# Performance work log

Hardware: AMD Instinct MI355X
Metric: run time of the kernel (lower is better)

## Reference

```python
import jax, jax.numpy as jnp
import numpy as np

NUM_LABELS = 10000
HIDDEN = 1024
B = 256
K = 4096


def setup_inputs() -> dict:
    key = jax.random.key(0)
    k1, k2, k3, k4, k5, k6 = jax.random.split(key, 6)
    embeddings = jax.random.normal(k1, (B, HIDDEN), dtype=jnp.float32)
    W1 = jax.random.normal(k2, (NUM_LABELS, 8, HIDDEN), dtype=jnp.float32) * 0.02
    b1 = jax.random.normal(k3, (NUM_LABELS, 8), dtype=jnp.float32) * 0.02
    W2 = jax.random.normal(k4, (NUM_LABELS, 1, 8), dtype=jnp.float32) * 0.02
    b2 = jax.random.normal(k5, (NUM_LABELS, 1), dtype=jnp.float32) * 0.02
    task_ids = jax.random.randint(k6, (K,), 0, NUM_LABELS, dtype=jnp.int64)
    return {"embeddings": embeddings, "W1": W1, "b1": b1, "W2": W2, "b2": b2, "task_ids": task_ids}


def reference(embeddings, W1, b1, W2, b2, task_ids):
    # Gather the selected heads (irregular access over the 10k-head tables).
    w1 = W1[task_ids]      # [K, 8, H]
    bb1 = b1[task_ids]     # [K, 8]
    w2 = W2[task_ids]      # [K, 1, 8]
    bb2 = b2[task_ids]     # [K, 1]
    # Batched tiny MLP: Linear(H,8) -> ReLU -> Linear(8,1), grouped over K heads.
    h = jax.nn.relu(jnp.einsum('bh,koh->kbo', embeddings, w1) + bb1[:, None, :])  # [K, B, 8]
    out = jnp.einsum('kbo,kio->kbi', h, w2) + bb2[:, None, :]                     # [K, B, 1]
    # torch: cat([head(emb).squeeze(-1) for ...], dim=-1) -> flat [K*B], task-major.
    return out[..., 0].reshape(-1)
```

## Files before the change

### kernel.cpp

```cpp
#include <hip/hip_runtime.h>

#define HID 1024
#define BATCH 256
#define KTASK 4096
#define TPB 8
#define NCOL (TPB * 8)
#define KC 32
#define NSTEPS (HID / KC)
#define STRIDE 80

typedef __bf16 bf16x8 __attribute__((ext_vector_type(8)));
typedef __bf16 bf16x4 __attribute__((ext_vector_type(4)));
typedef float f32x4 __attribute__((ext_vector_type(4)));

static __device__ __forceinline__ bf16x4 cvt4(const float4& a) {
    bf16x4 r;
    r[0] = (__bf16)a.x; r[1] = (__bf16)a.y; r[2] = (__bf16)a.z; r[3] = (__bf16)a.w;
    return r;
}

__global__ __launch_bounds__(256, 4)
void cvt_emb_kernel(const float* __restrict__ emb, __bf16* __restrict__ dst) {
    int i = (blockIdx.x * 256 + threadIdx.x) * 4;
    float4 v = *(const float4*)(emb + i);
    *(bf16x4*)(dst + i) = cvt4(v);
}

__global__ __launch_bounds__(512, 4)
void mtc_kernel(const __bf16* __restrict__ embb, const float* __restrict__ W1,
                const float* __restrict__ b1, const float* __restrict__ W2,
                const float* __restrict__ b2, const int* __restrict__ tids,
                float* __restrict__ out)
{
    __shared__ __align__(16) char wbuf[2][NCOL * STRIDE];

    const int t = threadIdx.x;
    const int lane = t & 63;
    const int w = t >> 6;
    const int blk = blockIdx.x;

    const int srow = t >> 3;
    const int sq   = t & 7;
    const int stask = tids[blk * TPB + (srow >> 3)];
    const float* sgp = W1 + (size_t)stask * (8 * HID) + (size_t)(srow & 7) * HID + sq * 4;
    char* const swr0 = &wbuf[0][0] + srow * STRIDE + sq * 8;
    char* const swr1 = swr0 + NCOL * STRIDE;

    const __bf16* agp = embb + (size_t)(w * 32 + (lane & 15)) * HID + (lane >> 4) * 8;
    const int boff = (lane & 15) * STRIDE + (lane >> 4) * 16;
    const char* const rb0 = &wbuf[0][0];
    const char* const rb1 = &wbuf[1][0];

    f32x4 acc[2][4];
    const f32x4 zero = {0.f, 0.f, 0.f, 0.f};
#pragma unroll
    for (int i = 0; i < 2; ++i)
#pragma unroll
        for (int j = 0; j < 4; ++j) acc[i][j] = zero;

    float4 wa = *(const float4*)(sgp);
    bf16x8 acur0 = *(const bf16x8*)(agp);
    bf16x8 acur1 = *(const bf16x8*)(agp + 16 * HID);
    *(bf16x4*)swr0 = cvt4(wa);
    float4 wb = *(const float4*)(sgp + KC);
    __syncthreads();

    for (int i = 0; i < 15; ++i) {
        const int s = 2 * i;
        {
            wa = *(const float4*)(sgp + (s + 2) * KC);
            bf16x8 an0 = *(const bf16x8*)(agp + (s + 1) * KC);
            bf16x8 an1 = *(const bf16x8*)(agp + (s + 1) * KC + 16 * HID);
#pragma unroll
            for (int nt = 0; nt < 4; ++nt) {
                bf16x8 bf = *(const bf16x8*)(rb0 + nt * (16 * STRIDE) + boff);
                acc[0][nt] = __builtin_amdgcn_mfma_f32_16x16x32_bf16(acur0, bf, acc[0][nt], 0, 0, 0);
                acc[1][nt] = __builtin_amdgcn_mfma_f32_16x16x32_bf16(acur1, bf, acc[1][nt], 0, 0, 0);
            }
            *(bf16x4*)swr1 = cvt4(wb);
            acur0 = an0; acur1 = an1;
            __syncthreads();
        }
        {
            wb = *(const float4*)(sgp + (s + 3) * KC);
            bf16x8 an0 = *(const bf16x8*)(agp + (s + 2) * KC);
            bf16x8 an1 = *(const bf16x8*)(agp + (s + 2) * KC + 16 * HID);
#pragma unroll
            for (int nt = 0; nt < 4; ++nt) {
                bf16x8 bf = *(const bf16x8*)(rb1 + nt * (16 * STRIDE) + boff);
                acc[0][nt] = __builtin_amdgcn_mfma_f32_16x16x32_bf16(acur0, bf, acc[0][nt], 0, 0, 0);
                acc[1][nt] = __builtin_amdgcn_mfma_f32_16x16x32_bf16(acur1, bf, acc[1][nt], 0, 0, 0);
            }
            *(bf16x4*)swr0 = cvt4(wa);
            acur0 = an0; acur1 = an1;
            __syncthreads();
        }
    }
    {
        bf16x8 an0 = *(const bf16x8*)(agp + 31 * KC);
        bf16x8 an1 = *(const bf16x8*)(agp + 31 * KC + 16 * HID);
#pragma unroll
        for (int nt = 0; nt < 4; ++nt) {
            bf16x8 bf = *(const bf16x8*)(rb0 + nt * (16 * STRIDE) + boff);
            acc[0][nt] = __builtin_amdgcn_mfma_f32_16x16x32_bf16(acur0, bf, acc[0][nt], 0, 0, 0);
            acc[1][nt] = __builtin_amdgcn_mfma_f32_16x16x32_bf16(acur1, bf, acc[1][nt], 0, 0, 0);
        }
        *(bf16x4*)swr1 = cvt4(wb);
        acur0 = an0; acur1 = an1;
        __syncthreads();
    }
    {
#pragma unroll
        for (int nt = 0; nt < 4; ++nt) {
            bf16x8 bf = *(const bf16x8*)(rb1 + nt * (16 * STRIDE) + boff);
            acc[0][nt] = __builtin_amdgcn_mfma_f32_16x16x32_bf16(acur0, bf, acc[0][nt], 0, 0, 0);
            acc[1][nt] = __builtin_amdgcn_mfma_f32_16x16x32_bf16(acur1, bf, acc[1][nt], 0, 0, 0);
        }
    }

    const int col = lane & 15;
    const int rgrp = lane >> 4;
    const int o = col & 7;
#pragma unroll
    for (int nt = 0; nt < 4; ++nt) {
        const int tl = nt * 2 + (col >> 3);
        const int task = tids[blk * TPB + tl];
        const float bb1 = b1[task * 8 + o];
        const float ww2 = W2[task * 8 + o];
#pragma unroll
        for (int bt = 0; bt < 2; ++bt) {
            float v[4];
#pragma unroll
            for (int r = 0; r < 4; ++r) {
                float x = acc[bt][nt][r] + bb1;
                x = x > 0.f ? x : 0.f;
                v[r] = x * ww2;
            }
#pragma unroll
            for (int m = 1; m <= 4; m <<= 1) {
#pragma unroll
                for (int r = 0; r < 4; ++r) v[r] += __shfl_xor(v[r], m, 64);
            }
            if ((lane & 7) == 0) {
                const float bb2 = b2[task];
                const int brow = w * 32 + bt * 16 + rgrp * 4;
                float4 o4 = make_float4(v[0] + bb2, v[1] + bb2, v[2] + bb2, v[3] + bb2);
                *(float4*)(out + (size_t)(blk * TPB + tl) * BATCH + brow) = o4;
            }
        }
    }
}

extern "C" void kernel_launch(void* const* d_in, const int* in_sizes, int n_in,
                              void* d_out, int out_size, void* d_ws, size_t ws_size,
                              hipStream_t stream) {
    const float* emb = (const float*)d_in[0];
    const float* W1  = (const float*)d_in[1];
    const float* b1  = (const float*)d_in[2];
    const float* W2  = (const float*)d_in[3];
    const float* b2  = (const float*)d_in[4];
    const int*   tid = (const int*)d_in[5];
    float* outp = (float*)d_out;
    __bf16* embb = (__bf16*)d_ws;

    cvt_emb_kernel<<<dim3(BATCH * HID / (256 * 4)), dim3(256), 0, stream>>>(emb, embb);
    mtc_kernel<<<dim3(KTASK / TPB), dim3(512), 0, stream>>>(embb, W1, b1, W2, b2, tid, outp);
}
```

Measured before the change: 50.09 us.

## Double K-chunk to 64 with triple-register prefetch pipeline for W1 staging

Widens each K step from 32 to 64 columns, halving the number of barriers and LDS stages, and has each thread load and convert 8 floats per step instead of 4. W1 global loads are now issued three steps ahead through a rotating set of three register buffers, and embedding fragments are loaded directly each step instead of being prefetched one step ahead. The aim is to expose more memory-level parallelism for the gathered W1 stream and cut synchronisation overhead. In exchange it needs more registers and a larger LDS footprint (144-byte stride), which could reduce occupancy.

```diff
diff --git a/kernel.cpp b/kernel.cpp
--- a/kernel.cpp
+++ b/kernel.cpp
@@ -4,18 +4,20 @@
 #define BATCH 256
 #define KTASK 4096
 #define TPB 8
-#define NCOL (TPB * 8)
-#define KC 32
-#define NSTEPS (HID / KC)
-#define STRIDE 80
+#define NCOL 64
+#define KC 64
+#define NSTEPS 16
+#define STRIDE 144
+#define BUFSZ (NCOL * STRIDE)
 
 typedef __bf16 bf16x8 __attribute__((ext_vector_type(8)));
 typedef __bf16 bf16x4 __attribute__((ext_vector_type(4)));
 typedef float f32x4 __attribute__((ext_vector_type(4)));
 
-static __device__ __forceinline__ bf16x4 cvt4(const float4& a) {
-    bf16x4 r;
+static __device__ __forceinline__ bf16x8 cvt8(const float4& a, const float4& b) {
+    bf16x8 r;
     r[0] = (__bf16)a.x; r[1] = (__bf16)a.y; r[2] = (__bf16)a.z; r[3] = (__bf16)a.w;
+    r[4] = (__bf16)b.x; r[5] = (__bf16)b.y; r[6] = (__bf16)b.z; r[7] = (__bf16)b.w;
     return r;
 }
 
@@ -23,7 +25,9 @@
 void cvt_emb_kernel(const float* __restrict__ emb, __bf16* __restrict__ dst) {
     int i = (blockIdx.x * 256 + threadIdx.x) * 4;
     float4 v = *(const float4*)(emb + i);
-    *(bf16x4*)(dst + i) = cvt4(v);
+    bf16x4 r;
+    r[0] = (__bf16)v.x; r[1] = (__bf16)v.y; r[2] = (__bf16)v.z; r[3] = (__bf16)v.w;
+    *(bf16x4*)(dst + i) = r;
 }
 
 __global__ __launch_bounds__(512, 4)
@@ -32,7 +36,7 @@
                 const float* __restrict__ b2, const int* __restrict__ tids,
                 float* __restrict__ out)
 {
-    __shared__ __align__(16) char wbuf[2][NCOL * STRIDE];
+    __shared__ __align__(16) char wbuf[2 * BUFSZ];
 
     const int t = threadIdx.x;
     const int lane = t & 63;
@@ -42,14 +46,11 @@
     const int srow = t >> 3;
     const int sq   = t & 7;
     const int stask = tids[blk * TPB + (srow >> 3)];
-    const float* sgp = W1 + (size_t)stask * (8 * HID) + (size_t)(srow & 7) * HID + sq * 4;
-    char* const swr0 = &wbuf[0][0] + srow * STRIDE + sq * 8;
-    char* const swr1 = swr0 + NCOL * STRIDE;
+    const float* sgp = W1 + (size_t)stask * (8 * HID) + (size_t)(srow & 7) * HID + sq * 8;
+    char* const swr = &wbuf[0] + srow * STRIDE + sq * 16;
 
     const __bf16* agp = embb + (size_t)(w * 32 + (lane & 15)) * HID + (lane >> 4) * 8;
     const int boff = (lane & 15) * STRIDE + (lane >> 4) * 16;
-    const char* const rb0 = &wbuf[0][0];
-    const char* const rb1 = &wbuf[1][0];
 
     f32x4 acc[2][4];
     const f32x4 zero = {0.f, 0.f, 0.f, 0.f};
@@ -58,65 +59,68 @@
 #pragma unroll
         for (int j = 0; j < 4; ++j) acc[i][j] = zero;
 
-    float4 wa = *(const float4*)(sgp);
-    bf16x8 acur0 = *(const bf16x8*)(agp);
-    bf16x8 acur1 = *(const bf16x8*)(agp + 16 * HID);
-    *(bf16x4*)swr0 = cvt4(wa);
-    float4 wb = *(const float4*)(sgp + KC);
+    float4 qa0 = *(const float4*)(sgp);
+    float4 qa1 = *(const float4*)(sgp + 4);
+    *(bf16x8*)swr = cvt8(qa0, qa1);
+    float4 qb0 = *(const float4*)(sgp + 1 * KC);
+    float4 qb1 = *(const float4*)(sgp + 1 * KC + 4);
+    float4 qc0 = *(const float4*)(sgp + 2 * KC);
+    float4 qc1 = *(const float4*)(sgp + 2 * KC + 4);
     __syncthreads();
 
-    for (int i = 0; i < 15; ++i) {
-        const int s = 2 * i;
-        {
-            wa = *(const float4*)(sgp + (s + 2) * KC);
-            bf16x8 an0 = *(const bf16x8*)(agp + (s + 1) * KC);
-            bf16x8 an1 = *(const bf16x8*)(agp + (s + 1) * KC + 16 * HID);
-#pragma unroll
-            for (int nt = 0; nt < 4; ++nt) {
-                bf16x8 bf = *(const bf16x8*)(rb0 + nt * (16 * STRIDE) + boff);
-                acc[0][nt] = __builtin_amdgcn_mfma_f32_16x16x32_bf16(acur0, bf, acc[0][nt], 0, 0, 0);
-                acc[1][nt] = __builtin_amdgcn_mfma_f32_16x16x32_bf16(acur1, bf, acc[1][nt], 0, 0, 0);
-            }
-            *(bf16x4*)swr1 = cvt4(wb);
-            acur0 = an0; acur1 = an1;
-            __syncthreads();
-        }
-        {
-            wb = *(const float4*)(sgp + (s + 3) * KC);
-            bf16x8 an0 = *(const bf16x8*)(agp + (s + 2) * KC);
-            bf16x8 an1 = *(const bf16x8*)(agp + (s + 2) * KC + 16 * HID);
-#pragma unroll
-            for (int nt = 0; nt < 4; ++nt) {
-                bf16x8 bf = *(const bf16x8*)(rb1 + nt * (16 * STRIDE) + boff);
-                acc[0][nt] = __builtin_amdgcn_mfma_f32_16x16x32_bf16(acur0, bf, acc[0][nt], 0, 0, 0);
-                acc[1][nt] = __builtin_amdgcn_mfma_f32_16x16x32_bf16(acur1, bf, acc[1][nt], 0, 0, 0);
-            }
-            *(bf16x4*)swr0 = cvt4(wa);
-            acur0 = an0; acur1 = an1;
-            __syncthreads();
-        }
+#define STEP(S, QW0, QW1, QI0, QI1, RB, WB, ISSUE, WRITE, BAR)                              \
+    {                                                                                       \
+        bf16x8 a00 = *(const bf16x8*)(agp + (S) * KC);                                      \
+        bf16x8 a01 = *(const bf16x8*)(agp + (S) * KC + 32);                                 \
+        bf16x8 a10 = *(const bf16x8*)(agp + (S) * KC + 16 * HID);                           \
+        bf16x8 a11 = *(const bf16x8*)(agp + (S) * KC + 16 * HID + 32);                      \
+        if (ISSUE) {                                                                        \
+            QI0 = *(const float4*)(sgp + ((S) + 3) * KC);                                   \
+            QI1 = *(const float4*)(sgp + ((S) + 3) * KC + 4);                               \
+        }                                                                                   \
+        const char* rb = &wbuf[0] + (RB) * BUFSZ;                                           \
+        bf16x8 b00 = *(const bf16x8*)(rb + 0 * (16 * STRIDE) + boff);                       \
+        bf16x8 b01 = *(const bf16x8*)(rb + 0 * (16 * STRIDE) + boff + 64);                  \
+        bf16x8 b10 = *(const bf16x8*)(rb + 1 * (16 * STRIDE) + boff);                       \
+        bf16x8 b11 = *(const bf16x8*)(rb + 1 * (16 * STRIDE) + boff + 64);                  \
+        bf16x8 b20 = *(const bf16x8*)(rb + 2 * (16 * STRIDE) + boff);                       \
+        bf16x8 b21 = *(const bf16x8*)(rb + 2 * (16 * STRIDE) + boff + 64);                  \
+        bf16x8 b30 = *(const bf16x8*)(rb + 3 * (16 * STRIDE) + boff);                       \
+        bf16x8 b31 = *(const bf16x8*)(rb + 3 * (16 * STRIDE) + boff + 64);                  \
+        if (WRITE) *(bf16x8*)(swr + (WB) * BUFSZ) = cvt8(QW0, QW1);                         \
+        acc[0][0] = __builtin_amdgcn_mfma_f32_16x16x32_bf16(a00, b00, acc[0][0], 0, 0, 0);  \
+        acc[0][1] = __builtin_amdgcn_mfma_f32_16x16x32_bf16(a00, b10, acc[0][1], 0, 0, 0);  \
+        acc[0][2] = __builtin_amdgcn_mfma_f32_16x16x32_bf16(a00, b20, acc[0][2], 0, 0, 0);  \
+        acc[0][3] = __builtin_amdgcn_mfma_f32_16x16x32_bf16(a00, b30, acc[0][3], 0, 0, 0);  \
+        acc[1][0] = __builtin_amdgcn_mfma_f32_16x16x32_bf16(a10, b00, acc[1][0], 0, 0, 0);  \
+        acc[1][1] = __builtin_amdgcn_mfma_f32_16x16x32_bf16(a10, b10, acc[1][1], 0, 0, 0);  \
+        acc[1][2] = __builtin_amdgcn_mfma_f32_16x16x32_bf16(a10, b20, acc[1][2], 0, 0, 0);  \
+        acc[1][3] = __builtin_amdgcn_mfma_f32_16x16x32_bf16(a10, b30, acc[1][3], 0, 0, 0);  \
+        acc[0][0] = __builtin_amdgcn_mfma_f32_16x16x32_bf16(a01, b01, acc[0][0], 0, 0, 0);  \
+        acc[0][1] = __builtin_amdgcn_mfma_f32_16x16x32_bf16(a01, b11, acc[0][1], 0, 0, 0);  \
+        acc[0][2] = __builtin_amdgcn_mfma_f32_16x16x32_bf16(a01, b21, acc[0][2], 0, 0, 0);  \
+        acc[0][3] = __builtin_amdgcn_mfma_f32_16x16x32_bf16(a01, b31, acc[0][3], 0, 0, 0);  \
+        acc[1][0] = __builtin_amdgcn_mfma_f32_16x16x32_bf16(a11, b01, acc[1][0], 0, 0, 0);  \
+        acc[1][1] = __builtin_amdgcn_mfma_f32_16x16x32_bf16(a11, b11, acc[1][1], 0, 0, 0);  \
+        acc[1][2] = __builtin_amdgcn_mfma_f32_16x16x32_bf16(a11, b21, acc[1][2], 0, 0, 0);  \
+        acc[1][3] = __builtin_amdgcn_mfma_f32_16x16x32_bf16(a11, b31, acc[1][3], 0, 0, 0);  \
+        if (BAR) __syncthreads();                                                           \
     }
-    {
-        bf16x8 an0 = *(const bf16x8*)(agp + 31 * KC);
-        bf16x8 an1 = *(const bf16x8*)(agp + 31 * KC + 16 * HID);
-#pragma unroll
-        for (int nt = 0; nt < 4; ++nt) {
-            bf16x8 bf = *(const bf16x8*)(rb0 + nt * (16 * STRIDE) + boff);
-            acc[0][nt] = __builtin_amdgcn_mfma_f32_16x16x32_bf16(acur0, bf, acc[0][nt], 0, 0, 0);
-            acc[1][nt] = __builtin_amdgcn_mfma_f32_16x16x32_bf16(acur1, bf, acc[1][nt], 0, 0, 0);
-        }
-        *(bf16x4*)swr1 = cvt4(wb);
-        acur0 = an0; acur1 = an1;
-        __syncthreads();
+
+    for (int i = 0; i < 2; ++i) {
+        const int s = 6 * i;
+        STEP(s + 0, qb0, qb1, qa0, qa1, 0, 1, 1, 1, 1)
+        STEP(s + 1, qc0, qc1, qb0, qb1, 1, 0, 1, 1, 1)
+        STEP(s + 2, qa0, qa1, qc0, qc1, 0, 1, 1, 1, 1)
+        STEP(s + 3, qb0, qb1, qa0, qa1, 1, 0, 1, 1, 1)
+        STEP(s + 4, qc0, qc1, qb0, qb1, 0, 1, 1, 1, 1)
+        STEP(s + 5, qa0, qa1, qc0, qc1, 1, 0, 1, 1, 1)
     }
-    {
-#pragma unroll
-        for (int nt = 0; nt < 4; ++nt) {
-            bf16x8 bf = *(const bf16x8*)(rb1 + nt * (16 * STRIDE) + boff);
-            acc[0][nt] = __builtin_amdgcn_mfma_f32_16x16x32_bf16(acur0, bf, acc[0][nt], 0, 0, 0);
-            acc[1][nt] = __builtin_amdgcn_mfma_f32_16x16x32_bf16(acur1, bf, acc[1][nt], 0, 0, 0);
-        }
-    }
+    STEP(12, qb0, qb1, qa0, qa1, 0, 1, 1, 1, 1)
+    STEP(13, qc0, qc1, qb0, qb1, 1, 0, 0, 1, 1)
+    STEP(14, qa0, qa1, qb0, qb1, 0, 1, 0, 1, 1)
+    STEP(15, qa0, qa1, qb0, qb1, 1, 0, 0, 0, 0)
+#undef STEP
 
     const int col = lane & 15;
     const int rgrp = lane >> 4;
```

Measured after the change: 52.59 us. 5.0% more time.

## Stage whole per-block weight slice in LDS upfront, halve tasks per block

Applied to the files above, without the earlier changes.

Each block now handles 4 tasks instead of 8. It loads all of their W1 rows (32 rows by 1024) with 16 independent float4 loads per thread, converts them to bf16 and stores them in padded LDS, then syncs once. The K loop then runs fully unrolled with no barriers, reading B fragments from LDS and double-buffering only the embedding fragments. This removes the 32 per-step barriers and the serialized weight-streaming pipeline, but the block grid doubles, so each embedding tile is reloaded twice as often. It also uses about 66KB of LDS per block, which limits occupancy.

```diff
diff --git a/kernel.cpp b/kernel.cpp
--- a/kernel.cpp
+++ b/kernel.cpp
@@ -3,27 +3,21 @@
 #define HID 1024
 #define BATCH 256
 #define KTASK 4096
-#define TPB 8
-#define NCOL (TPB * 8)
-#define KC 32
-#define NSTEPS (HID / KC)
-#define STRIDE 80
+#define TPB 4
+#define NCOL 32
+#define WSTRIDE 2064
 
 typedef __bf16 bf16x8 __attribute__((ext_vector_type(8)));
 typedef __bf16 bf16x4 __attribute__((ext_vector_type(4)));
 typedef float f32x4 __attribute__((ext_vector_type(4)));
 
-static __device__ __forceinline__ bf16x4 cvt4(const float4& a) {
-    bf16x4 r;
-    r[0] = (__bf16)a.x; r[1] = (__bf16)a.y; r[2] = (__bf16)a.z; r[3] = (__bf16)a.w;
-    return r;
-}
-
 __global__ __launch_bounds__(256, 4)
 void cvt_emb_kernel(const float* __restrict__ emb, __bf16* __restrict__ dst) {
     int i = (blockIdx.x * 256 + threadIdx.x) * 4;
     float4 v = *(const float4*)(emb + i);
-    *(bf16x4*)(dst + i) = cvt4(v);
+    bf16x4 r;
+    r[0] = (__bf16)v.x; r[1] = (__bf16)v.y; r[2] = (__bf16)v.z; r[3] = (__bf16)v.w;
+    *(bf16x4*)(dst + i) = r;
 }
 
 __global__ __launch_bounds__(512, 4)
@@ -32,89 +26,80 @@
                 const float* __restrict__ b2, const int* __restrict__ tids,
                 float* __restrict__ out)
 {
-    __shared__ __align__(16) char wbuf[2][NCOL * STRIDE];
+    __shared__ __align__(16) char wlds[NCOL * WSTRIDE];
 
     const int t = threadIdx.x;
     const int lane = t & 63;
     const int w = t >> 6;
     const int blk = blockIdx.x;
 
-    const int srow = t >> 3;
-    const int sq   = t & 7;
-    const int stask = tids[blk * TPB + (srow >> 3)];
-    const float* sgp = W1 + (size_t)stask * (8 * HID) + (size_t)(srow & 7) * HID + sq * 4;
-    char* const swr0 = &wbuf[0][0] + srow * STRIDE + sq * 8;
-    char* const swr1 = swr0 + NCOL * STRIDE;
+    int tk[TPB];
+#pragma unroll
+    for (int i = 0; i < TPB; ++i) tk[i] = tids[blk * TPB + i];
+
+    {
+        float4 v[16];
+#pragma unroll
+        for (int j = 0; j < 16; ++j) {
+            const int f = t + j * 512;
+            const int tl = j >> 2;
+            const float* p = W1 + (size_t)tk[tl] * (8 * HID) + (size_t)(f & 2047) * 4;
+            v[j] = *(const float4*)p;
+        }
+#pragma unroll
+        for (int j = 0; j < 16; ++j) {
+            const int f = t + j * 512;
+            const int row = f >> 8;
+            const int q   = f & 255;
+            bf16x4 r;
+            r[0] = (__bf16)v[j].x; r[1] = (__bf16)v[j].y;
+            r[2] = (__bf16)v[j].z; r[3] = (__bf16)v[j].w;
+            *(bf16x4*)(&wlds[0] + row * WSTRIDE + q * 8) = r;
+        }
+    }
+    __syncthreads();
 
     const __bf16* agp = embb + (size_t)(w * 32 + (lane & 15)) * HID + (lane >> 4) * 8;
-    const int boff = (lane & 15) * STRIDE + (lane >> 4) * 16;
-    const char* const rb0 = &wbuf[0][0];
-    const char* const rb1 = &wbuf[1][0];
+    const char* b0p = &wlds[0] + (lane & 15) * WSTRIDE + (lane >> 4) * 16;
+    const char* b1p = b0p + 16 * WSTRIDE;
 
-    f32x4 acc[2][4];
+    f32x4 acc[2][2];
     const f32x4 zero = {0.f, 0.f, 0.f, 0.f};
 #pragma unroll
     for (int i = 0; i < 2; ++i)
 #pragma unroll
-        for (int j = 0; j < 4; ++j) acc[i][j] = zero;
+        for (int j = 0; j < 2; ++j) acc[i][j] = zero;
 
-    float4 wa = *(const float4*)(sgp);
-    bf16x8 acur0 = *(const bf16x8*)(agp);
-    bf16x8 acur1 = *(const bf16x8*)(agp + 16 * HID);
-    *(bf16x4*)swr0 = cvt4(wa);
-    float4 wb = *(const float4*)(sgp + KC);
-    __syncthreads();
+    bf16x8 aA0 = *(const bf16x8*)(agp);
+    bf16x8 aA1 = *(const bf16x8*)(agp + 16 * HID);
+    bf16x8 aB0 = *(const bf16x8*)(agp + 32);
+    bf16x8 aB1 = *(const bf16x8*)(agp + 32 + 16 * HID);
 
-    for (int i = 0; i < 15; ++i) {
-        const int s = 2 * i;
+#pragma unroll
+    for (int s = 0; s < 32; s += 2) {
         {
-            wa = *(const float4*)(sgp + (s + 2) * KC);
-            bf16x8 an0 = *(const bf16x8*)(agp + (s + 1) * KC);
-            bf16x8 an1 = *(const bf16x8*)(agp + (s + 1) * KC + 16 * HID);
-#pragma unroll
-            for (int nt = 0; nt < 4; ++nt) {
-                bf16x8 bf = *(const bf16x8*)(rb0 + nt * (16 * STRIDE) + boff);
-                acc[0][nt] = __builtin_amdgcn_mfma_f32_16x16x32_bf16(acur0, bf, acc[0][nt], 0, 0, 0);
-                acc[1][nt] = __builtin_amdgcn_mfma_f32_16x16x32_bf16(acur1, bf, acc[1][nt], 0, 0, 0);
+            bf16x8 bf0 = *(const bf16x8*)(b0p + s * 64);
+            bf16x8 bf1 = *(const bf16x8*)(b1p + s * 64);
+            acc[0][0] = __builtin_amdgcn_mfma_f32_16x16x32_bf16(aA0, bf0, acc[0][0], 0, 0, 0);
+            acc[0][1] = __builtin_amdgcn_mfma_f32_16x16x32_bf16(aA0, bf1, acc[0][1], 0, 0, 0);
+            acc[1][0] = __builtin_amdgcn_mfma_f32_16x16x32_bf16(aA1, bf0, acc[1][0], 0, 0, 0);
+            acc[1][1] = __builtin_amdgcn_mfma_f32_16x16x32_bf16(aA1, bf1, acc[1][1], 0, 0, 0);
+            if (s + 2 < 32) {
+                aA0 = *(const bf16x8*)(agp + (s + 2) * 32);
+                aA1 = *(const bf16x8*)(agp + (s + 2) * 32 + 16 * HID);
             }
-            *(bf16x4*)swr1 = cvt4(wb);
-            acur0 = an0; acur1 = an1;
-            __syncthreads();
         }
         {
-            wb = *(const float4*)(sgp + (s + 3) * KC);
-            bf16x8 an0 = *(const bf16x8*)(agp + (s + 2) * KC);
-            bf16x8 an1 = *(const bf16x8*)(agp + (s + 2) * KC + 16 * HID);
-#pragma unroll
-            for (int nt = 0; nt < 4; ++nt) {
-                bf16x8 bf = *(const bf16x8*)(rb1 + nt * (16 * STRIDE) + boff);
-                acc[0][nt] = __builtin_amdgcn_mfma_f32_16x16x32_bf16(acur0, bf, acc[0][nt], 0, 0, 0);
-                acc[1][nt] = __builtin_amdgcn_mfma_f32_16x16x32_bf16(acur1, bf, acc[1][nt], 0, 0, 0);
+            bf16x8 bf0 = *(const bf16x8*)(b0p + (s + 1) * 64);
+            bf16x8 bf1 = *(const bf16x8*)(b1p + (s + 1) * 64);
+            acc[0][0] = __builtin_amdgcn_mfma_f32_16x16x32_bf16(aB0, bf0, acc[0][0], 0, 0, 0);
+            acc[0][1] = __builtin_amdgcn_mfma_f32_16x16x32_bf16(aB0, bf1, acc[0][1], 0, 0, 0);
+            acc[1][0] = __builtin_amdgcn_mfma_f32_16x16x32_bf16(aB1, bf0, acc[1][0], 0, 0, 0);
+            acc[1][1] = __builtin_amdgcn_mfma_f32_16x16x32_bf16(aB1, bf1, acc[1][1], 0, 0, 0);
+            if (s + 3 < 32) {
+                aB0 = *(const bf16x8*)(agp + (s + 3) * 32);
+                aB1 = *(const bf16x8*)(agp + (s + 3) * 32 + 16 * HID);
             }
-            *(bf16x4*)swr0 = cvt4(wa);
-            acur0 = an0; acur1 = an1;
-            __syncthreads();
-        }
-    }
-    {
-        bf16x8 an0 = *(const bf16x8*)(agp + 31 * KC);
-        bf16x8 an1 = *(const bf16x8*)(agp + 31 * KC + 16 * HID);
-#pragma unroll
-        for (int nt = 0; nt < 4; ++nt) {
-            bf16x8 bf = *(const bf16x8*)(rb0 + nt * (16 * STRIDE) + boff);
-            acc[0][nt] = __builtin_amdgcn_mfma_f32_16x16x32_bf16(acur0, bf, acc[0][nt], 0, 0, 0);
-            acc[1][nt] = __builtin_amdgcn_mfma_f32_16x16x32_bf16(acur1, bf, acc[1][nt], 0, 0, 0);
-        }
-        *(bf16x4*)swr1 = cvt4(wb);
-        acur0 = an0; acur1 = an1;
-        __syncthreads();
-    }
-    {
-#pragma unroll
-        for (int nt = 0; nt < 4; ++nt) {
-            bf16x8 bf = *(const bf16x8*)(rb1 + nt * (16 * STRIDE) + boff);
-            acc[0][nt] = __builtin_amdgcn_mfma_f32_16x16x32_bf16(acur0, bf, acc[0][nt], 0, 0, 0);
-            acc[1][nt] = __builtin_amdgcn_mfma_f32_16x16x32_bf16(acur1, bf, acc[1][nt], 0, 0, 0);
         }
     }
 
@@ -122,17 +107,19 @@
     const int rgrp = lane >> 4;
     const int o = col & 7;
 #pragma unroll
-    for (int nt = 0; nt < 4; ++nt) {
+    for (int nt = 0; nt < 2; ++nt) {
         const int tl = nt * 2 + (col >> 3);
-        const int task = tids[blk * TPB + tl];
-        const float bb1 = b1[task * 8 + o];
-        const float ww2 = W2[task * 8 + o];
+        const int task = tk[0];
+        const int task_r = (tl == 0) ? tk[0] : (tl == 1) ? tk[1] : (tl == 2) ? tk[2] : tk[3];
+        (void)task;
+        const float bb1 = b1[task_r * 8 + o];
+        const float ww2 = W2[task_r * 8 + o];
 #pragma unroll
-        for (int bt = 0; bt < 2; ++bt) {
+        for (int mt = 0; mt < 2; ++mt) {
             float v[4];
 #pragma unroll
             for (int r = 0; r < 4; ++r) {
-                float x = acc[bt][nt][r] + bb1;
+                float x = acc[mt][nt][r] + bb1;
                 x = x > 0.f ? x : 0.f;
                 v[r] = x * ww2;
             }
@@ -142,8 +129,8 @@
                 for (int r = 0; r < 4; ++r) v[r] += __shfl_xor(v[r], m, 64);
             }
             if ((lane & 7) == 0) {
-                const float bb2 = b2[task];
-                const int brow = w * 32 + bt * 16 + rgrp * 4;
+                const float bb2 = b2[task_r];
+                const int brow = w * 32 + mt * 16 + rgrp * 4;
                 float4 o4 = make_float4(v[0] + bb2, v[1] + bb2, v[2] + bb2, v[3] + bb2);
                 *(float4*)(out + (size_t)(blk * TPB + tl) * BATCH + brow) = o4;
             }
```

New measurement: 82.88 us. 65.5% more time.

## Deepen W1 gather pipeline to four LDS stages with register prefetch

Applied to the files above, without the earlier changes.

Replaces the double-buffered LDS pipeline with a 4-stage ring buffer. Global W1 loads are issued four steps ahead and embedding loads two steps ahead, which keeps more memory requests in flight to hide gather latency. Barriers become raw s_barrier with an explicit lgkmcnt wait, and sched_barrier pins the order of loads relative to the MFMAs. This costs more LDS and more registers per thread, which could limit occupancy at 4 blocks per CU.

```diff
diff --git a/kernel.cpp b/kernel.cpp
--- a/kernel.cpp
+++ b/kernel.cpp
@@ -4,10 +4,10 @@
 #define BATCH 256
 #define KTASK 4096
 #define TPB 8
-#define NCOL (TPB * 8)
+#define NCOL 64
 #define KC 32
-#define NSTEPS (HID / KC)
 #define STRIDE 80
+#define BUFSZ (NCOL * STRIDE)
 
 typedef __bf16 bf16x8 __attribute__((ext_vector_type(8)));
 typedef __bf16 bf16x4 __attribute__((ext_vector_type(4)));
@@ -32,7 +32,7 @@
                 const float* __restrict__ b2, const int* __restrict__ tids,
                 float* __restrict__ out)
 {
-    __shared__ __align__(16) char wbuf[2][NCOL * STRIDE];
+    __shared__ __align__(16) char wbuf[4 * BUFSZ];
 
     const int t = threadIdx.x;
     const int lane = t & 63;
@@ -43,13 +43,10 @@
     const int sq   = t & 7;
     const int stask = tids[blk * TPB + (srow >> 3)];
     const float* sgp = W1 + (size_t)stask * (8 * HID) + (size_t)(srow & 7) * HID + sq * 4;
-    char* const swr0 = &wbuf[0][0] + srow * STRIDE + sq * 8;
-    char* const swr1 = swr0 + NCOL * STRIDE;
+    char* const swr = &wbuf[0] + srow * STRIDE + sq * 8;
 
     const __bf16* agp = embb + (size_t)(w * 32 + (lane & 15)) * HID + (lane >> 4) * 8;
     const int boff = (lane & 15) * STRIDE + (lane >> 4) * 16;
-    const char* const rb0 = &wbuf[0][0];
-    const char* const rb1 = &wbuf[1][0];
 
     f32x4 acc[2][4];
     const f32x4 zero = {0.f, 0.f, 0.f, 0.f};
@@ -58,65 +55,62 @@
 #pragma unroll
         for (int j = 0; j < 4; ++j) acc[i][j] = zero;
 
-    float4 wa = *(const float4*)(sgp);
-    bf16x8 acur0 = *(const bf16x8*)(agp);
-    bf16x8 acur1 = *(const bf16x8*)(agp + 16 * HID);
-    *(bf16x4*)swr0 = cvt4(wa);
-    float4 wb = *(const float4*)(sgp + KC);
-    __syncthreads();
+    bf16x8 aS[4][2];
+    float4 wS[4];
 
-    for (int i = 0; i < 15; ++i) {
-        const int s = 2 * i;
-        {
-            wa = *(const float4*)(sgp + (s + 2) * KC);
-            bf16x8 an0 = *(const bf16x8*)(agp + (s + 1) * KC);
-            bf16x8 an1 = *(const bf16x8*)(agp + (s + 1) * KC + 16 * HID);
-#pragma unroll
-            for (int nt = 0; nt < 4; ++nt) {
-                bf16x8 bf = *(const bf16x8*)(rb0 + nt * (16 * STRIDE) + boff);
-                acc[0][nt] = __builtin_amdgcn_mfma_f32_16x16x32_bf16(acur0, bf, acc[0][nt], 0, 0, 0);
-                acc[1][nt] = __builtin_amdgcn_mfma_f32_16x16x32_bf16(acur1, bf, acc[1][nt], 0, 0, 0);
-            }
-            *(bf16x4*)swr1 = cvt4(wb);
-            acur0 = an0; acur1 = an1;
-            __syncthreads();
-        }
-        {
-            wb = *(const float4*)(sgp + (s + 3) * KC);
-            bf16x8 an0 = *(const bf16x8*)(agp + (s + 2) * KC);
-            bf16x8 an1 = *(const bf16x8*)(agp + (s + 2) * KC + 16 * HID);
-#pragma unroll
-            for (int nt = 0; nt < 4; ++nt) {
-                bf16x8 bf = *(const bf16x8*)(rb1 + nt * (16 * STRIDE) + boff);
-                acc[0][nt] = __builtin_amdgcn_mfma_f32_16x16x32_bf16(acur0, bf, acc[0][nt], 0, 0, 0);
-                acc[1][nt] = __builtin_amdgcn_mfma_f32_16x16x32_bf16(acur1, bf, acc[1][nt], 0, 0, 0);
-            }
-            *(bf16x4*)swr0 = cvt4(wa);
-            acur0 = an0; acur1 = an1;
-            __syncthreads();
-        }
+    aS[0][0] = *(const bf16x8*)(agp);
+    aS[0][1] = *(const bf16x8*)(agp + 16 * HID);
+    aS[1][0] = *(const bf16x8*)(agp + KC);
+    aS[1][1] = *(const bf16x8*)(agp + KC + 16 * HID);
+    wS[0] = *(const float4*)(sgp);
+    wS[1] = *(const float4*)(sgp + 1 * KC);
+    wS[2] = *(const float4*)(sgp + 2 * KC);
+    wS[3] = *(const float4*)(sgp + 3 * KC);
+    *(bf16x4*)(swr + 0 * BUFSZ) = cvt4(wS[0]);
+    *(bf16x4*)(swr + 1 * BUFSZ) = cvt4(wS[1]);
+    asm volatile("s_waitcnt lgkmcnt(0)" ::: "memory");
+    __builtin_amdgcn_s_barrier();
+
+#define STEP(S, P, ISSA, ISSW, WRT, BAR)                                                    \
+    {                                                                                       \
+        if (ISSA) {                                                                         \
+            aS[((P) + 2) & 3][0] = *(const bf16x8*)(agp + ((S) + 2) * KC);                  \
+            aS[((P) + 2) & 3][1] = *(const bf16x8*)(agp + ((S) + 2) * KC + 16 * HID);       \
+        }                                                                                   \
+        if (ISSW) wS[(P)] = *(const float4*)(sgp + ((S) + 4) * KC);                         \
+        __builtin_amdgcn_sched_barrier(0);                                                  \
+        const char* rb = &wbuf[0] + (P) * BUFSZ;                                            \
+        bf16x8 b0 = *(const bf16x8*)(rb + 0 * (16 * STRIDE) + boff);                        \
+        bf16x8 b1 = *(const bf16x8*)(rb + 1 * (16 * STRIDE) + boff);                        \
+        bf16x8 b2 = *(const bf16x8*)(rb + 2 * (16 * STRIDE) + boff);                        \
+        bf16x8 b3 = *(const bf16x8*)(rb + 3 * (16 * STRIDE) + boff);                        \
+        acc[0][0] = __builtin_amdgcn_mfma_f32_16x16x32_bf16(aS[P][0], b0, acc[0][0], 0, 0, 0); \
+        acc[0][1] = __builtin_amdgcn_mfma_f32_16x16x32_bf16(aS[P][0], b1, acc[0][1], 0, 0, 0); \
+        acc[0][2] = __builtin_amdgcn_mfma_f32_16x16x32_bf16(aS[P][0], b2, acc[0][2], 0, 0, 0); \
+        acc[0][3] = __builtin_amdgcn_mfma_f32_16x16x32_bf16(aS[P][0], b3, acc[0][3], 0, 0, 0); \
+        acc[1][0] = __builtin_amdgcn_mfma_f32_16x16x32_bf16(aS[P][1], b0, acc[1][0], 0, 0, 0); \
+        acc[1][1] = __builtin_amdgcn_mfma_f32_16x16x32_bf16(aS[P][1], b1, acc[1][1], 0, 0, 0); \
+        acc[1][2] = __builtin_amdgcn_mfma_f32_16x16x32_bf16(aS[P][1], b2, acc[1][2], 0, 0, 0); \
+        acc[1][3] = __builtin_amdgcn_mfma_f32_16x16x32_bf16(aS[P][1], b3, acc[1][3], 0, 0, 0); \
+        if (WRT) *(bf16x4*)(swr + (((P) + 2) & 3) * BUFSZ) = cvt4(wS[((P) + 2) & 3]);       \
+        if (BAR) {                                                                          \
+            asm volatile("s_waitcnt lgkmcnt(0)" ::: "memory");                              \
+            __builtin_amdgcn_s_barrier();                                                   \
+        }                                                                                   \
     }
-    {
-        bf16x8 an0 = *(const bf16x8*)(agp + 31 * KC);
-        bf16x8 an1 = *(const bf16x8*)(agp + 31 * KC + 16 * HID);
-#pragma unroll
-        for (int nt = 0; nt < 4; ++nt) {
-            bf16x8 bf = *(const bf16x8*)(rb0 + nt * (16 * STRIDE) + boff);
-            acc[0][nt] = __builtin_amdgcn_mfma_f32_16x16x32_bf16(acur0, bf, acc[0][nt], 0, 0, 0);
-            acc[1][nt] = __builtin_amdgcn_mfma_f32_16x16x32_bf16(acur1, bf, acc[1][nt], 0, 0, 0);
-        }
-        *(bf16x4*)swr1 = cvt4(wb);
-        acur0 = an0; acur1 = an1;
-        __syncthreads();
+
+    for (int ii = 0; ii < 7; ++ii) {
+        const int s = ii * 4;
+        STEP(s + 0, 0, 1, 1, 1, 1)
+        STEP(s + 1, 1, 1, 1, 1, 1)
+        STEP(s + 2, 2, 1, 1, 1, 1)
+        STEP(s + 3, 3, 1, 1, 1, 1)
     }
-    {
-#pragma unroll
-        for (int nt = 0; nt < 4; ++nt) {
-            bf16x8 bf = *(const bf16x8*)(rb1 + nt * (16 * STRIDE) + boff);
-            acc[0][nt] = __builtin_amdgcn_mfma_f32_16x16x32_bf16(acur0, bf, acc[0][nt], 0, 0, 0);
-            acc[1][nt] = __builtin_amdgcn_mfma_f32_16x16x32_bf16(acur1, bf, acc[1][nt], 0, 0, 0);
-        }
-    }
+    STEP(28, 0, 1, 0, 1, 1)
+    STEP(29, 1, 1, 0, 1, 1)
+    STEP(30, 2, 0, 0, 0, 0)
+    STEP(31, 3, 0, 0, 0, 0)
+#undef STEP
 
     const int col = lane & 15;
     const int rgrp = lane >> 4;
```

After: 59.11 us. 18.0% more time.
